# Kernel optimization log

Hardware: AMD Instinct MI355X
Metric: run time of the kernel (lower is better)

## Reference

```python
import jax, jax.numpy as jnp
import numpy as np

B, P, ENC = 128, 196, 2048
A, E, H = 512, 512, 512
V, TMAX = 20000, 20


def setup_inputs() -> dict:
    key = jax.random.key(0)
    ks = jax.random.split(key, 16)
    s = 0.02
    img = jax.random.normal(ks[0], (B, P, ENC), jnp.float32)
    cap = jax.random.randint(ks[1], (B, TMAX), 0, V)
    # ensure max(caplen) == TMAX so output shapes are deterministic
    caplen = jnp.concatenate([jnp.array([TMAX]),
                              jax.random.randint(ks[2], (B - 1,), 5, TMAX + 1)])
    emb = s * jax.random.normal(ks[3], (V, E), jnp.float32)
    We = s * jax.random.normal(ks[4], (ENC, A), jnp.float32)
    be = jnp.zeros((A,), jnp.float32)
    Wd = s * jax.random.normal(ks[5], (H, A), jnp.float32)
    bd = jnp.zeros((A,), jnp.float32)
    Wf = s * jax.random.normal(ks[6], (A, 1), jnp.float32)
    bf = jnp.zeros((1,), jnp.float32)
    W_ih = s * jax.random.normal(ks[7], (3 * H, E + ENC), jnp.float32)
    b_ih = jnp.zeros((3 * H,), jnp.float32)
    W_hh = s * jax.random.normal(ks[8], (3 * H, H), jnp.float32)
    b_hh = jnp.zeros((3 * H,), jnp.float32)
    Wo = s * jax.random.normal(ks[9], (V, H), jnp.float32)
    bo = jnp.zeros((V,), jnp.float32)
    return dict(img=img, cap=cap, caplen=caplen, emb=emb, We=We, be=be,
                Wd=Wd, bd=bd, Wf=Wf, bf=bf, W_ih=W_ih, b_ih=b_ih,
                W_hh=W_hh, b_hh=b_hh, Wo=Wo, bo=bo)


def reference(img, cap, caplen, emb, We, be, Wd, bd, Wf, bf,
              W_ih, b_ih, W_hh, b_hh, Wo, bo):
    T = int(np.asarray(jnp.max(caplen)))  # static loop length (caplen.tolist() in torch)
    word_emb = emb[cap]                       # [B, TMAX, E]
    att1 = jnp.einsum('bpe,ea->bpa', img, We) + be  # encoder attention, hoisted (img is constant over steps)

    def step(h, x_t):
        att2 = h @ Wd + bd                    # [B, A]
        fatt = jax.nn.relu(att1 + att2[:, None, :])   # [B, P, A]
        scores = fatt @ Wf + bf               # [B, P, 1]
        alpha = jax.nn.softmax(scores, axis=1)        # softmax over pixels
        ctx = jnp.sum(alpha * img, axis=1)    # [B, ENC]
        x = jnp.concatenate([x_t, ctx], axis=1)       # [B, E+ENC]
        gi = x @ W_ih.T + b_ih                # [B, 3H]
        gh = h @ W_hh.T + b_hh
        r = jax.nn.sigmoid(gi[:, :H] + gh[:, :H])
        z = jax.nn.sigmoid(gi[:, H:2 * H] + gh[:, H:2 * H])
        n = jnp.tanh(gi[:, 2 * H:] + r * gh[:, 2 * H:])
        h_new = (1.0 - z) * n + z * h
        preds = h_new @ Wo.T + bo             # [B, V]
        return h_new, (preds, alpha[..., 0])

    h0 = jnp.zeros((B, H), jnp.float32)
    xs = jnp.swapaxes(word_emb[:, :T - 1, :], 0, 1)   # [T-1, B, E]; step i uses word_emb[:, i-1]
    _, (preds_seq, alpha_seq) = jax.lax.scan(step, h0, xs)

    predictions = jnp.zeros((B, T, V), jnp.float32)
    predictions = predictions.at[:, 1:, :].set(jnp.swapaxes(preds_seq, 0, 1))
    predictions = predictions.at[:, 0, 1].set(1.0)
    alphas = jnp.zeros((B, T, P), jnp.float32)
    alphas = alphas.at[:, 1:, :].set(jnp.swapaxes(alpha_seq, 0, 1))
    return predictions, caplen, alphas
```

## Files before the change

### kernel.cpp

```cpp
#include <hip/hip_runtime.h>
#include <hip/hip_bf16.h>

#define B_    128
#define P_    196
#define ENC_  2048
#define A_    512
#define E_    512
#define H_    512
#define V_    20000
#define TMAX_ 20

#define CAPLEN_OFF 51200000L
#define ALPHA_OFF  51200128L

typedef __attribute__((ext_vector_type(4))) float f32x4;
typedef __attribute__((ext_vector_type(8))) short bf16x8;

#define GLL16(gsrc, ldst) \
  __builtin_amdgcn_global_load_lds((__attribute__((address_space(1))) const void*)(gsrc), \
                                   (__attribute__((address_space(3))) void*)(ldst), 16, 0, 0)

__device__ __forceinline__ unsigned short f2b(float x) {
  union { float f; unsigned u; } v; v.f = x;
  unsigned r = v.u + 0x7FFF + ((v.u >> 16) & 1);
  return (unsigned short)(r >> 16);
}
__device__ __forceinline__ float b2f(unsigned short u) {
  union { unsigned u; float f; } v; v.u = ((unsigned)u) << 16; return v.f;
}

__global__ __launch_bounds__(256) void k_setup(const int* __restrict__ caplen,
                                               float* __restrict__ out,
                                               float* __restrict__ h,
                                               unsigned short* __restrict__ h_bf) {
  long idx = (long)blockIdx.x * 256 + threadIdx.x;
  if (idx < (long)B_ * V_) {
    long b = idx / V_, v = idx % V_;
    out[b * (long)TMAX_ * V_ + v] = (v == 1) ? 1.0f : 0.0f;
  }
  if (idx < B_) out[CAPLEN_OFF + idx] = (float)caplen[idx];
  if (idx < (long)B_ * P_) {
    long b = idx / P_, p = idx % P_;
    out[ALPHA_OFF + b * (long)(TMAX_ * P_) + p] = 0.0f;
  }
  if (idx < B_ * H_) { h[idx] = 0.0f; h_bf[idx] = 0; }
}

__global__ __launch_bounds__(256) void k_cvt_t(const float* __restrict__ src,
                                               unsigned short* __restrict__ dst,
                                               int R, int C) {
  __shared__ float tile[32][33];
  int lx = threadIdx.x & 31, ly = threadIdx.x >> 5;
  int r0 = blockIdx.x * 32, c0 = blockIdx.y * 32;
#pragma unroll
  for (int j = 0; j < 32; j += 8)
    tile[ly + j][lx] = src[(long)(r0 + ly + j) * C + c0 + lx];
  __syncthreads();
#pragma unroll
  for (int j = 0; j < 32; j += 8)
    dst[(long)(c0 + ly + j) * R + r0 + lx] = f2b(tile[lx][ly + j]);
}

__global__ __launch_bounds__(256) void k_cvt_wo(const float* __restrict__ Wo,
                                                unsigned short* __restrict__ Wo_bf) {
  long gid = (long)blockIdx.x * 256 + threadIdx.x;
  long base = gid * 8;
  if (base >= (long)20096 * 512) return;
  long row = base >> 9;
  bf16x8 u;
  if (row < V_) {
    float4 f0 = *(const float4*)(Wo + base);
    float4 f1 = *(const float4*)(Wo + base + 4);
    u[0] = (short)f2b(f0.x); u[1] = (short)f2b(f0.y);
    u[2] = (short)f2b(f0.z); u[3] = (short)f2b(f0.w);
    u[4] = (short)f2b(f1.x); u[5] = (short)f2b(f1.y);
    u[6] = (short)f2b(f1.z); u[7] = (short)f2b(f1.w);
  } else {
    for (int j = 0; j < 8; ++j) u[j] = 0;
  }
  *(bf16x8*)(Wo_bf + base) = u;
}

__global__ __launch_bounds__(256) void k_cvt_img(const float* __restrict__ img,
                                                 unsigned short* __restrict__ img_bf) {
  long base = ((long)blockIdx.x * 256 + threadIdx.x) * 8;
  float4 f0 = *(const float4*)(img + base);
  float4 f1 = *(const float4*)(img + base + 4);
  bf16x8 u;
  u[0] = (short)f2b(f0.x); u[1] = (short)f2b(f0.y);
  u[2] = (short)f2b(f0.z); u[3] = (short)f2b(f0.w);
  u[4] = (short)f2b(f1.x); u[5] = (short)f2b(f1.y);
  u[6] = (short)f2b(f1.z); u[7] = (short)f2b(f1.w);
  *(bf16x8*)(img_bf + base) = u;
}

__global__ __launch_bounds__(256) void k_mfma_nt(const unsigned short* __restrict__ Abf,
                                                 const unsigned short* __restrict__ Bbf,
                                                 const float* __restrict__ bias,
                                                 float* __restrict__ C, long ldc,
                                                 int N, int K) {
  __shared__ unsigned short As[4096];
  __shared__ unsigned short Bs[4096];
  int tid = threadIdx.x, wave = tid >> 6, lane = tid & 63;
  int m0 = blockIdx.x * 128, n0 = blockIdx.y * 128;
  int wm = (wave & 1) * 64, wn = (wave >> 1) * 64;
  int rowL = tid >> 2, chkL = (tid & 3) * 8;
  const unsigned short* gA0 = Abf + (long)(m0 + rowL) * K + chkL;
  const unsigned short* gA1 = gA0 + (long)64 * K;
  const unsigned short* gB0 = Bbf + (long)(n0 + rowL) * K + chkL;
  const unsigned short* gB1 = gB0 + (long)64 * K;
  unsigned short* ldsA = As + wave * 512;
  unsigned short* ldsB = Bs + wave * 512;

  f32x4 acc[4][4];
#pragma unroll
  for (int i = 0; i < 4; ++i)
#pragma unroll
    for (int j = 0; j < 4; ++j) acc[i][j] = (f32x4){0.f, 0.f, 0.f, 0.f};

  int fm = lane & 15, q8 = (lane >> 4) * 8;
  for (int kc = 0; kc < K; kc += 32) {
    GLL16(gA0 + kc, ldsA);
    GLL16(gA1 + kc, ldsA + 2048);
    GLL16(gB0 + kc, ldsB);
    GLL16(gB1 + kc, ldsB + 2048);
    __syncthreads();
    bf16x8 af[4], bfr[4];
#pragma unroll
    for (int i = 0; i < 4; ++i)
      af[i] = *(const bf16x8*)&As[(wm + i * 16 + fm) * 32 + q8];
#pragma unroll
    for (int j = 0; j < 4; ++j)
      bfr[j] = *(const bf16x8*)&Bs[(wn + j * 16 + fm) * 32 + q8];
#pragma unroll
    for (int i = 0; i < 4; ++i)
#pragma unroll
      for (int j = 0; j < 4; ++j)
        acc[i][j] = __builtin_amdgcn_mfma_f32_16x16x32_bf16(af[i], bfr[j], acc[i][j], 0, 0, 0);
    __syncthreads();
  }
  int q4 = (lane >> 4) * 4;
#pragma unroll
  for (int i = 0; i < 4; ++i)
#pragma unroll
    for (int j = 0; j < 4; ++j) {
      int n = n0 + wn + j * 16 + fm;
      if (n < N) {
        float bv = bias[n];
#pragma unroll
        for (int r = 0; r < 4; ++r) {
          long m = m0 + wm + i * 16 + q4 + r;
          C[m * ldc + n] = acc[i][j][r] + bv;
        }
      }
    }
}

__global__ __launch_bounds__(256) void k_mfma_att1(const float* __restrict__ Aimg,
                                                   const unsigned short* __restrict__ Bbf,
                                                   const float* __restrict__ bias,
                                                   unsigned short* __restrict__ C) {
  __shared__ unsigned short As[4096];
  __shared__ unsigned short Bs[4096];
  int tid = threadIdx.x, wave = tid >> 6, lane = tid & 63;
  int m0 = blockIdx.x * 128, n0 = blockIdx.y * 128;
  int wm = (wave & 1) * 64, wn = (wave >> 1) * 64;
  int rowA = tid >> 1, segA = (tid & 1) * 16;
  const float* gA = Aimg + (long)(m0 + rowA) * ENC_ + segA;
  int rowL = tid >> 2, chkL = (tid & 3) * 8;
  const unsigned short* gB0 = Bbf + (long)(n0 + rowL) * ENC_ + chkL;
  const unsigned short* gB1 = gB0 + (long)64 * ENC_;
  unsigned short* ldsB = Bs + wave * 512;

  f32x4 acc[4][4];
#pragma unroll
  for (int i = 0; i < 4; ++i)
#pragma unroll
    for (int j = 0; j < 4; ++j) acc[i][j] = (f32x4){0.f, 0.f, 0.f, 0.f};

  int fm = lane & 15, q8 = (lane >> 4) * 8;
  for (int kc = 0; kc < ENC_; kc += 32) {
    GLL16(gB0 + kc, ldsB);
    GLL16(gB1 + kc, ldsB + 2048);
    float4 f0 = *(const float4*)(gA + kc);
    float4 f1 = *(const float4*)(gA + kc + 4);
    float4 f2 = *(const float4*)(gA + kc + 8);
    float4 f3 = *(const float4*)(gA + kc + 12);
    bf16x8 u0, u1;
    u0[0] = (short)f2b(f0.x); u0[1] = (short)f2b(f0.y);
    u0[2] = (short)f2b(f0.z); u0[3] = (short)f2b(f0.w);
    u0[4] = (short)f2b(f1.x); u0[5] = (short)f2b(f1.y);
    u0[6] = (short)f2b(f1.z); u0[7] = (short)f2b(f1.w);
    u1[0] = (short)f2b(f2.x); u1[1] = (short)f2b(f2.y);
    u1[2] = (short)f2b(f2.z); u1[3] = (short)f2b(f2.w);
    u1[4] = (short)f2b(f3.x); u1[5] = (short)f2b(f3.y);
    u1[6] = (short)f2b(f3.z); u1[7] = (short)f2b(f3.w);
    *(bf16x8*)&As[rowA * 32 + segA] = u0;
    *(bf16x8*)&As[rowA * 32 + segA + 8] = u1;
    __syncthreads();
    bf16x8 af[4], bfr[4];
#pragma unroll
    for (int i = 0; i < 4; ++i)
      af[i] = *(const bf16x8*)&As[(wm + i * 16 + fm) * 32 + q8];
#pragma unroll
    for (int j = 0; j < 4; ++j)
      bfr[j] = *(const bf16x8*)&Bs[(wn + j * 16 + fm) * 32 + q8];
#pragma unroll
    for (int i = 0; i < 4; ++i)
#pragma unroll
      for (int j = 0; j < 4; ++j)
        acc[i][j] = __builtin_amdgcn_mfma_f32_16x16x32_bf16(af[i], bfr[j], acc[i][j], 0, 0, 0);
    __syncthreads();
  }
  int q4 = (lane >> 4) * 4;
#pragma unroll
  for (int i = 0; i < 4; ++i)
#pragma unroll
    for (int j = 0; j < 4; ++j) {
      int n = n0 + wn + j * 16 + fm;
      float bv = bias[n];
#pragma unroll
      for (int r = 0; r < 4; ++r) {
        long m = m0 + wm + i * 16 + q4 + r;
        C[m * 512 + n] = f2b(acc[i][j][r] + bv);
      }
    }
}

__global__ __launch_bounds__(256) void k_attn_score(const unsigned short* __restrict__ att1_bf,
                                                    const float* __restrict__ att2,
                                                    const float* __restrict__ Wf,
                                                    const float* __restrict__ bfp,
                                                    float* __restrict__ alpha_ws,
                                                    float* __restrict__ out_alpha,
                                                    int t) {
  int b = blockIdx.x, tid = threadIdx.x;
  int wave = tid >> 6, lane = tid & 63;
  __shared__ float sc[P_ + 4];
  __shared__ float red[8];

  float a2[8], w8[8];
  {
    const float* ap = att2 + (long)b * 512 + lane * 8;
    float4 x0 = *(const float4*)ap, x1 = *(const float4*)(ap + 4);
    a2[0] = x0.x; a2[1] = x0.y; a2[2] = x0.z; a2[3] = x0.w;
    a2[4] = x1.x; a2[5] = x1.y; a2[6] = x1.z; a2[7] = x1.w;
    const float* wp = Wf + lane * 8;
    float4 y0 = *(const float4*)wp, y1 = *(const float4*)(wp + 4);
    w8[0] = y0.x; w8[1] = y0.y; w8[2] = y0.z; w8[3] = y0.w;
    w8[4] = y1.x; w8[5] = y1.y; w8[6] = y1.z; w8[7] = y1.w;
  }
  float bias0 = bfp[0];

  for (int p = wave; p < P_; p += 4) {
    bf16x8 v = *(const bf16x8*)(att1_bf + ((long)(b * P_ + p)) * 512 + lane * 8);
    float part = 0.f;
#pragma unroll
    for (int j = 0; j < 8; ++j) {
      float x = b2f((unsigned short)v[j]) + a2[j];
      part = fmaf(fmaxf(x, 0.f), w8[j], part);
    }
#pragma unroll
    for (int off = 32; off > 0; off >>= 1) part += __shfl_down(part, off);
    if (lane == 0) sc[p] = part + bias0;
  }
  __syncthreads();

  float mv = (tid < P_) ? sc[tid] : -1e30f;
#pragma unroll
  for (int off = 32; off > 0; off >>= 1) mv = fmaxf(mv, __shfl_down(mv, off));
  if (lane == 0) red[wave] = mv;
  __syncthreads();
  if (tid == 0) red[4] = fmaxf(fmaxf(red[0], red[1]), fmaxf(red[2], red[3]));
  __syncthreads();
  float mx = red[4];
  float e = (tid < P_) ? __expf(sc[tid] - mx) : 0.f;
  float sm = e;
#pragma unroll
  for (int off = 32; off > 0; off >>= 1) sm += __shfl_down(sm, off);
  if (lane == 0) red[wave] = sm;
  __syncthreads();
  if (tid == 0) red[5] = red[0] + red[1] + red[2] + red[3];
  __syncthreads();
  float inv = 1.f / red[5];
  if (tid < P_) {
    float al = e * inv;
    alpha_ws[b * P_ + tid] = al;
    out_alpha[((long)b * TMAX_ + t) * P_ + tid] = al;
  }
}

template <bool BFIMG>
__global__ __launch_bounds__(256) void k_attn_ctx(const void* __restrict__ img_v,
                                                  const float* __restrict__ alpha_ws,
                                                  float* __restrict__ ctx) {
  int b = blockIdx.x, ec = blockIdx.y;
  int tid = threadIdx.x, wave = tid >> 6, lane = tid & 63;
  __shared__ float als[P_];
  __shared__ float part[4][512];
  if (tid < P_) als[tid] = alpha_ws[b * P_ + tid];
  __syncthreads();
  float acc[8];
#pragma unroll
  for (int j = 0; j < 8; ++j) acc[j] = 0.f;
  long base = (long)b * P_ * ENC_ + ec * 512 + lane * 8;
  if (BFIMG) {
    const unsigned short* ib = (const unsigned short*)img_v;
    for (int p = wave; p < P_; p += 4) {
      float al = als[p];
      bf16x8 v = *(const bf16x8*)(ib + base + (long)p * ENC_);
#pragma unroll
      for (int j = 0; j < 8; ++j) acc[j] = fmaf(al, b2f((unsigned short)v[j]), acc[j]);
    }
  } else {
    const float* ip = (const float*)img_v;
    for (int p = wave; p < P_; p += 4) {
      float al = als[p];
      const float* r = ip + base + (long)p * ENC_;
      float4 v0 = *(const float4*)r, v1 = *(const float4*)(r + 4);
      acc[0] = fmaf(al, v0.x, acc[0]); acc[1] = fmaf(al, v0.y, acc[1]);
      acc[2] = fmaf(al, v0.z, acc[2]); acc[3] = fmaf(al, v0.w, acc[3]);
      acc[4] = fmaf(al, v1.x, acc[4]); acc[5] = fmaf(al, v1.y, acc[5]);
      acc[6] = fmaf(al, v1.z, acc[6]); acc[7] = fmaf(al, v1.w, acc[7]);
    }
  }
#pragma unroll
  for (int j = 0; j < 8; ++j) part[wave][lane * 8 + j] = acc[j];
  __syncthreads();
  for (int e = tid; e < 512; e += 256) {
    float s = part[0][e] + part[1][e] + part[2][e] + part[3][e];
    ctx[(long)b * ENC_ + ec * 512 + e] = s;
  }
}

__global__ __launch_bounds__(256) void k_gru_part(const float* __restrict__ emb,
                                                  const int* __restrict__ cap,
                                                  const float* __restrict__ ctx,
                                                  const float* __restrict__ h,
                                                  const float* __restrict__ W_ih,
                                                  const float* __restrict__ W_hh,
                                                  float* __restrict__ part,
                                                  int step) {
  __shared__ float As[128][68];
  __shared__ float Ws[32][68];
  int n0 = blockIdx.x * 32;
  int c  = blockIdx.y;
  int tid = threadIdx.x;
  int ng = tid & 7, mg = tid >> 3;

  float acc[4][4];
#pragma unroll
  for (int i = 0; i < 4; ++i)
#pragma unroll
    for (int j = 0; j < 4; ++j) acc[i][j] = 0.f;

  const float* Wbase;
  long wstride;
  if (c < 10) { Wbase = W_ih + (long)n0 * 2560 + c * 256;        wstride = 2560; }
  else        { Wbase = W_hh + (long)n0 * 512 + (c - 10) * 256;  wstride = 512;  }

  for (int s = 0; s < 4; ++s) {
    int ks = s * 64;
#pragma unroll
    for (int j = 0; j < 8; ++j) {
      int f = tid + j * 256;
      int r = f >> 4, kk = (f & 15) * 4;
      const float* src;
      if (c < 2)       src = emb + (long)cap[r * TMAX_ + step] * E_ + c * 256 + ks + kk;
      else if (c < 10) src = ctx + (long)r * ENC_ + (c - 2) * 256 + ks + kk;
      else             src = h   + (long)r * H_   + (c - 10) * 256 + ks + kk;
      *(float4*)&As[r][kk] = *(const float4*)src;
    }
#pragma unroll
    for (int j = 0; j < 2; ++j) {
      int f = tid + j * 256;
      int r = f >> 4, kk = (f & 15) * 4;
      *(float4*)&Ws[r][kk] = *(const float4*)(Wbase + (long)r * wstride + ks + kk);
    }
    __syncthreads();
#pragma unroll 4
    for (int k4 = 0; k4 < 16; ++k4) {
      float4 a[4], w[4];
#pragma unroll
      for (int i = 0; i < 4; ++i) a[i] = *(const float4*)&As[mg + 32 * i][k4 * 4];
#pragma unroll
      for (int j = 0; j < 4; ++j) w[j] = *(const float4*)&Ws[ng + 8 * j][k4 * 4];
#pragma unroll
      for (int i = 0; i < 4; ++i)
#pragma unroll
        for (int j = 0; j < 4; ++j)
          acc[i][j] = fmaf(a[i].x, w[j].x,
                      fmaf(a[i].y, w[j].y,
                      fmaf(a[i].z, w[j].z,
                      fmaf(a[i].w, w[j].w, acc[i][j]))));
    }
    __syncthreads();
  }

  float* dst = part + (long)c * (128 * 1536);
#pragma unroll
  for (int i = 0; i < 4; ++i) {
    int m = mg + 32 * i;
#pragma unroll
    for (int j = 0; j < 4; ++j)
      dst[(long)m * 1536 + n0 + ng + 8 * j] = acc[i][j];
  }
}

__global__ __launch_bounds__(256) void k_gate2(const float* __restrict__ part,
                                               const float* __restrict__ b_ih,
                                               const float* __restrict__ b_hh,
                                               float* __restrict__ h,
                                               unsigned short* __restrict__ h_bf) {
  int idx = blockIdx.x * 256 + threadIdx.x;
  int b = idx >> 9, j = idx & 511;
  long o = (long)b * 1536 + j;
  const long PS = 128L * 1536;
  float gir = 0.f, giz = 0.f, gin = 0.f;
  float ghr = 0.f, ghz = 0.f, ghn = 0.f;
#pragma unroll
  for (int c = 0; c < 10; ++c) {
    gir += part[c * PS + o];
    giz += part[c * PS + o + 512];
    gin += part[c * PS + o + 1024];
  }
#pragma unroll
  for (int c = 10; c < 12; ++c) {
    ghr += part[c * PS + o];
    ghz += part[c * PS + o + 512];
    ghn += part[c * PS + o + 1024];
  }
  gir += b_ih[j];        ghr += b_hh[j];
  giz += b_ih[j + 512];  ghz += b_hh[j + 512];
  gin += b_ih[j + 1024]; ghn += b_hh[j + 1024];
  float r = 1.f / (1.f + __expf(-(gir + ghr)));
  float z = 1.f / (1.f + __expf(-(giz + ghz)));
  float nn = tanhf(gin + r * ghn);
  float hv = h[idx];
  float v = (1.f - z) * nn + z * hv;
  h[idx] = v;
  h_bf[idx] = f2b(v);
}

__global__ __launch_bounds__(256) void k_gru_gemm(const float* __restrict__ emb,
                                                  const int* __restrict__ cap,
                                                  const float* __restrict__ ctx,
                                                  const float* __restrict__ h,
                                                  const float* __restrict__ W_ih,
                                                  const float* __restrict__ b_ih,
                                                  const float* __restrict__ W_hh,
                                                  const float* __restrict__ b_hh,
                                                  float* __restrict__ gi,
                                                  float* __restrict__ gh,
                                                  int step) {
  __shared__ float As[32][256];
  int m0 = blockIdx.x * 32;
  int n0 = blockIdx.y * 64;
  int tid = threadIdx.x;
  int np = tid & 31, slot = tid >> 5;
  int n = n0 + np * 2;
  float ai[4][2], ah[4][2];
#pragma unroll
  for (int i = 0; i < 4; ++i) { ai[i][0] = ai[i][1] = ah[i][0] = ah[i][1] = 0.f; }

  for (int c = 0; c < 10; ++c) {
#pragma unroll
    for (int j = 0; j < 8; ++j) {
      int f = tid + j * 256;
      int r = f >> 6, k = (f & 63) * 4;
      int bb = m0 + r;
      const float* src;
      if (c < 2) src = emb + (long)cap[bb * TMAX_ + step] * E_ + c * 256 + k;
      else       src = ctx + (long)bb * ENC_ + (c - 2) * 256 + k;
      *(float4*)&As[r][k] = *(const float4*)src;
    }
    __syncthreads();
    const float* W0 = W_ih + (long)n * 2560 + c * 256;
    const float* W1 = W0 + 2560;
#pragma unroll 4
    for (int k4 = 0; k4 < 64; ++k4) {
      float4 b0 = *(const float4*)&W0[k4 * 4];
      float4 b1 = *(const float4*)&W1[k4 * 4];
#pragma unroll
      for (int i = 0; i < 4; ++i) {
        float4 a = *(const float4*)&As[slot * 4 + i][k4 * 4];
        ai[i][0] = fmaf(a.x, b0.x, fmaf(a.y, b0.y, fmaf(a.z, b0.z, fmaf(a.w, b0.w, ai[i][0]))));
        ai[i][1] = fmaf(a.x, b1.x, fmaf(a.y, b1.y, fmaf(a.z, b1.z, fmaf(a.w, b1.w, ai[i][1]))));
      }
    }
    __syncthreads();
  }
  for (int c = 0; c < 2; ++c) {
#pragma unroll
    for (int j = 0; j < 8; ++j) {
      int f = tid + j * 256;
      int r = f >> 6, k = (f & 63) * 4;
      int bb = m0 + r;
      *(float4*)&As[r][k] = *(const float4*)&h[(long)bb * H_ + c * 256 + k];
    }
    __syncthreads();
    const float* W0 = W_hh + (long)n * 512 + c * 256;
    const float* W1 = W0 + 512;
#pragma unroll 4
    for (int k4 = 0; k4 < 64; ++k4) {
      float4 b0 = *(const float4*)&W0[k4 * 4];
      float4 b1 = *(const float4*)&W1[k4 * 4];
#pragma unroll
      for (int i = 0; i < 4; ++i) {
        float4 a = *(const float4*)&As[slot * 4 + i][k4 * 4];
        ah[i][0] = fmaf(a.x, b0.x, fmaf(a.y, b0.y, fmaf(a.z, b0.z, fmaf(a.w, b0.w, ah[i][0]))));
        ah[i][1] = fmaf(a.x, b1.x, fmaf(a.y, b1.y, fmaf(a.z, b1.z, fmaf(a.w, b1.w, ah[i][1]))));
      }
    }
    __syncthreads();
  }
#pragma unroll
  for (int i = 0; i < 4; ++i) {
    long m = m0 + slot * 4 + i;
    gi[m * 1536 + n]     = ai[i][0] + b_ih[n];
    gi[m * 1536 + n + 1] = ai[i][1] + b_ih[n + 1];
    gh[m * 1536 + n]     = ah[i][0] + b_hh[n];
    gh[m * 1536 + n + 1] = ah[i][1] + b_hh[n + 1];
  }
}

__global__ __launch_bounds__(256) void k_gate(const float* __restrict__ gi,
                                              const float* __restrict__ gh,
                                              float* __restrict__ h,
                                              unsigned short* __restrict__ h_bf) {
  int idx = blockIdx.x * 256 + threadIdx.x;
  int b = idx >> 9, j = idx & 511;
  long o = (long)b * 1536 + j;
  float r = 1.f / (1.f + __expf(-(gi[o] + gh[o])));
  float z = 1.f / (1.f + __expf(-(gi[o + 512] + gh[o + 512])));
  float nn = tanhf(gi[o + 1024] + r * gh[o + 1024]);
  float hv = h[idx];
  float v = (1.f - z) * nn + z * hv;
  h[idx] = v;
  h_bf[idx] = f2b(v);
}

extern "C" void kernel_launch(void* const* d_in, const int* in_sizes, int n_in,
                              void* d_out, int out_size, void* d_ws, size_t ws_size,
                              hipStream_t stream) {
  const float* img    = (const float*)d_in[0];
  const int*   cap    = (const int*)d_in[1];
  const int*   caplen = (const int*)d_in[2];
  const float* emb    = (const float*)d_in[3];
  const float* We     = (const float*)d_in[4];
  const float* be     = (const float*)d_in[5];
  const float* Wd     = (const float*)d_in[6];
  const float* bd     = (const float*)d_in[7];
  const float* Wf     = (const float*)d_in[8];
  const float* bfp    = (const float*)d_in[9];
  const float* W_ih   = (const float*)d_in[10];
  const float* b_ih   = (const float*)d_in[11];
  const float* W_hh   = (const float*)d_in[12];
  const float* b_hh   = (const float*)d_in[13];
  const float* Wo     = (const float*)d_in[14];
  const float* bo     = (const float*)d_in[15];
  float* out = (float*)d_out;
  char*  W   = (char*)d_ws;

  unsigned short* att1_bf = (unsigned short*)(W + 0);
  unsigned short* WeT_bf  = (unsigned short*)(W + 25690112);
  unsigned short* WdT_bf  = (unsigned short*)(W + 27787264);
  unsigned short* Wo_bf   = (unsigned short*)(W + 28311552);
  float*          h       = (float*)(W + 48889856);
  unsigned short* h_bf    = (unsigned short*)(W + 49152000);
  float*          ctx     = (float*)(W + 49283072);
  float*          gi      = (float*)(W + 50331648);
  float*          gh      = (float*)(W + 51118080);
  float*          att2    = (float*)(W + 51904512);
  float*          alpha_w = (float*)(W + 52166656);
  unsigned short* img_bf  = (unsigned short*)(W + 52267008);
  float*          part    = (float*)(W + 155027456);
  bool use_bfimg = ws_size >= 155027456ULL;
  bool use_part  = ws_size >= 164464640ULL;

  k_setup<<<10000, 256, 0, stream>>>(caplen, out, h, h_bf);
  k_cvt_t<<<dim3(64, 16), 256, 0, stream>>>(We, WeT_bf, ENC_, A_);
  k_cvt_t<<<dim3(16, 16), 256, 0, stream>>>(Wd, WdT_bf, H_, A_);
  k_cvt_wo<<<5024, 256, 0, stream>>>(Wo, Wo_bf);
  if (use_bfimg) k_cvt_img<<<25088, 256, 0, stream>>>(img, img_bf);
  k_mfma_att1<<<dim3(196, 4), 256, 0, stream>>>(img, WeT_bf, be, att1_bf);

  for (int i = 0; i < TMAX_ - 1; ++i) {
    int t = i + 1;
    k_mfma_nt<<<dim3(1, 4), 256, 0, stream>>>(h_bf, WdT_bf, bd, att2, 512, 512, 512);
    k_attn_score<<<128, 256, 0, stream>>>(att1_bf, att2, Wf, bfp, alpha_w,
                                          out + ALPHA_OFF, t);
    if (use_bfimg)
      k_attn_ctx<true><<<dim3(128, 4), 256, 0, stream>>>(img_bf, alpha_w, ctx);
    else
      k_attn_ctx<false><<<dim3(128, 4), 256, 0, stream>>>(img, alpha_w, ctx);
    if (use_part) {
      k_gru_part<<<dim3(48, 12), 256, 0, stream>>>(emb, cap, ctx, h, W_ih, W_hh,
                                                   part, i);
      k_gate2<<<256, 256, 0, stream>>>(part, b_ih, b_hh, h, h_bf);
    } else {
      k_gru_gemm<<<dim3(4, 24), 256, 0, stream>>>(emb, cap, ctx, h, W_ih, b_ih,
                                                  W_hh, b_hh, gi, gh, i);
      k_gate<<<256, 256, 0, stream>>>(gi, gh, h, h_bf);
    }
    k_mfma_nt<<<dim3(1, 157), 256, 0, stream>>>(h_bf, Wo_bf, bo,
                                                out + (long)t * V_,
                                                (long)TMAX_ * V_, V_, 512);
  }
}
```

Baseline: 2.871 ms.

## Split attention context over pixel chunks with atomics; reuse bf16 GEMM for att1

The attention-context kernel now splits the 196 pixels into 7 chunks of 28. Each block accumulates its partial context and adds it into ctx with atomics. ctx is zeroed inside the score kernel, so more blocks are in flight and no per-block shared-memory reduction is needed. When the bf16 image copy exists, the att1 projection now runs through the generic bf16 GEMM with a templated bf16 output instead of the kernel that converts fp32 on the fly. The fallback GRU gemm/gate path, which lacked the partial-sum workspace, is removed. The changes risk atomic contention, nondeterministic summation order, and breakage when the workspace is too small for the partial buffer.

```diff
diff --git a/kernel.cpp b/kernel.cpp
--- a/kernel.cpp
+++ b/kernel.cpp
@@ -94,10 +94,11 @@
   *(bf16x8*)(img_bf + base) = u;
 }
 
-__global__ __launch_bounds__(256) void k_mfma_nt(const unsigned short* __restrict__ Abf,
+template <int OBF>
+__global__ __launch_bounds__(256) void k_gemm_nt(const unsigned short* __restrict__ Abf,
                                                  const unsigned short* __restrict__ Bbf,
                                                  const float* __restrict__ bias,
-                                                 float* __restrict__ C, long ldc,
+                                                 void* __restrict__ Cv, long ldc,
                                                  int N, int K) {
   __shared__ unsigned short As[4096];
   __shared__ unsigned short Bs[4096];
@@ -146,11 +147,12 @@
     for (int j = 0; j < 4; ++j) {
       int n = n0 + wn + j * 16 + fm;
       if (n < N) {
-        float bv = bias[n];
+        float bv = bias ? bias[n] : 0.f;
 #pragma unroll
         for (int r = 0; r < 4; ++r) {
           long m = m0 + wm + i * 16 + q4 + r;
-          C[m * ldc + n] = acc[i][j][r] + bv;
+          if (OBF) ((unsigned short*)Cv)[m * ldc + n] = f2b(acc[i][j][r] + bv);
+          else     ((float*)Cv)[m * ldc + n] = acc[i][j][r] + bv;
         }
       }
     }
@@ -233,11 +235,19 @@
                                                     const float* __restrict__ bfp,
                                                     float* __restrict__ alpha_ws,
                                                     float* __restrict__ out_alpha,
+                                                    float* __restrict__ ctx,
                                                     int t) {
   int b = blockIdx.x, tid = threadIdx.x;
   int wave = tid >> 6, lane = tid & 63;
   __shared__ float sc[P_ + 4];
   __shared__ float red[8];
+
+  {
+    float4 z4 = {0.f, 0.f, 0.f, 0.f};
+    float* c = ctx + (long)b * ENC_ + tid * 8;
+    *(float4*)c = z4;
+    *(float4*)(c + 4) = z4;
+  }
 
   float a2[8], w8[8];
   {
@@ -290,8 +300,31 @@
   }
 }
 
-template <bool BFIMG>
-__global__ __launch_bounds__(256) void k_attn_ctx(const void* __restrict__ img_v,
+__global__ __launch_bounds__(256) void k_attn_ctx2(const unsigned short* __restrict__ img_bf,
+                                                   const float* __restrict__ alpha_ws,
+                                                   float* __restrict__ ctx) {
+  int b = blockIdx.x, pc = blockIdx.y;
+  int tid = threadIdx.x;
+  __shared__ float als[28];
+  if (tid < 28) als[tid] = alpha_ws[b * P_ + pc * 28 + tid];
+  __syncthreads();
+  float acc[8];
+#pragma unroll
+  for (int j = 0; j < 8; ++j) acc[j] = 0.f;
+  const unsigned short* base = img_bf + ((long)b * P_ + pc * 28) * ENC_ + tid * 8;
+#pragma unroll 4
+  for (int p = 0; p < 28; ++p) {
+    bf16x8 v = *(const bf16x8*)(base + (long)p * ENC_);
+    float al = als[p];
+#pragma unroll
+    for (int j = 0; j < 8; ++j) acc[j] = fmaf(al, b2f((unsigned short)v[j]), acc[j]);
+  }
+  float* c = ctx + (long)b * ENC_ + tid * 8;
+#pragma unroll
+  for (int j = 0; j < 8; ++j) atomicAdd(c + j, acc[j]);
+}
+
+__global__ __launch_bounds__(256) void k_attn_ctx(const float* __restrict__ img,
                                                   const float* __restrict__ alpha_ws,
                                                   float* __restrict__ ctx) {
   int b = blockIdx.x, ec = blockIdx.y;
@@ -304,25 +337,14 @@
 #pragma unroll
   for (int j = 0; j < 8; ++j) acc[j] = 0.f;
   long base = (long)b * P_ * ENC_ + ec * 512 + lane * 8;
-  if (BFIMG) {
-    const unsigned short* ib = (const unsigned short*)img_v;
-    for (int p = wave; p < P_; p += 4) {
-      float al = als[p];
-      bf16x8 v = *(const bf16x8*)(ib + base + (long)p * ENC_);
-#pragma unroll
-      for (int j = 0; j < 8; ++j) acc[j] = fmaf(al, b2f((unsigned short)v[j]), acc[j]);
-    }
-  } else {
-    const float* ip = (const float*)img_v;
-    for (int p = wave; p < P_; p += 4) {
-      float al = als[p];
-      const float* r = ip + base + (long)p * ENC_;
-      float4 v0 = *(const float4*)r, v1 = *(const float4*)(r + 4);
-      acc[0] = fmaf(al, v0.x, acc[0]); acc[1] = fmaf(al, v0.y, acc[1]);
-      acc[2] = fmaf(al, v0.z, acc[2]); acc[3] = fmaf(al, v0.w, acc[3]);
-      acc[4] = fmaf(al, v1.x, acc[4]); acc[5] = fmaf(al, v1.y, acc[5]);
-      acc[6] = fmaf(al, v1.z, acc[6]); acc[7] = fmaf(al, v1.w, acc[7]);
-    }
+  for (int p = wave; p < P_; p += 4) {
+    float al = als[p];
+    const float* r = img + base + (long)p * ENC_;
+    float4 v0 = *(const float4*)r, v1 = *(const float4*)(r + 4);
+    acc[0] = fmaf(al, v0.x, acc[0]); acc[1] = fmaf(al, v0.y, acc[1]);
+    acc[2] = fmaf(al, v0.z, acc[2]); acc[3] = fmaf(al, v0.w, acc[3]);
+    acc[4] = fmaf(al, v1.x, acc[4]); acc[5] = fmaf(al, v1.y, acc[5]);
+    acc[6] = fmaf(al, v1.z, acc[6]); acc[7] = fmaf(al, v1.w, acc[7]);
   }
 #pragma unroll
   for (int j = 0; j < 8; ++j) part[wave][lane * 8 + j] = acc[j];
@@ -436,104 +458,6 @@
   float r = 1.f / (1.f + __expf(-(gir + ghr)));
   float z = 1.f / (1.f + __expf(-(giz + ghz)));
   float nn = tanhf(gin + r * ghn);
-  float hv = h[idx];
-  float v = (1.f - z) * nn + z * hv;
-  h[idx] = v;
-  h_bf[idx] = f2b(v);
-}
-
-__global__ __launch_bounds__(256) void k_gru_gemm(const float* __restrict__ emb,
-                                                  const int* __restrict__ cap,
-                                                  const float* __restrict__ ctx,
-                                                  const float* __restrict__ h,
-                                                  const float* __restrict__ W_ih,
-                                                  const float* __restrict__ b_ih,
-                                                  const float* __restrict__ W_hh,
-                                                  const float* __restrict__ b_hh,
-                                                  float* __restrict__ gi,
-                                                  float* __restrict__ gh,
-                                                  int step) {
-  __shared__ float As[32][256];
-  int m0 = blockIdx.x * 32;
-  int n0 = blockIdx.y * 64;
-  int tid = threadIdx.x;
-  int np = tid & 31, slot = tid >> 5;
-  int n = n0 + np * 2;
-  float ai[4][2], ah[4][2];
-#pragma unroll
-  for (int i = 0; i < 4; ++i) { ai[i][0] = ai[i][1] = ah[i][0] = ah[i][1] = 0.f; }
-
-  for (int c = 0; c < 10; ++c) {
-#pragma unroll
-    for (int j = 0; j < 8; ++j) {
-      int f = tid + j * 256;
-      int r = f >> 6, k = (f & 63) * 4;
-      int bb = m0 + r;
-      const float* src;
-      if (c < 2) src = emb + (long)cap[bb * TMAX_ + step] * E_ + c * 256 + k;
-      else       src = ctx + (long)bb * ENC_ + (c - 2) * 256 + k;
-      *(float4*)&As[r][k] = *(const float4*)src;
-    }
-    __syncthreads();
-    const float* W0 = W_ih + (long)n * 2560 + c * 256;
-    const float* W1 = W0 + 2560;
-#pragma unroll 4
-    for (int k4 = 0; k4 < 64; ++k4) {
-      float4 b0 = *(const float4*)&W0[k4 * 4];
-      float4 b1 = *(const float4*)&W1[k4 * 4];
-#pragma unroll
-      for (int i = 0; i < 4; ++i) {
-        float4 a = *(const float4*)&As[slot * 4 + i][k4 * 4];
-        ai[i][0] = fmaf(a.x, b0.x, fmaf(a.y, b0.y, fmaf(a.z, b0.z, fmaf(a.w, b0.w, ai[i][0]))));
-        ai[i][1] = fmaf(a.x, b1.x, fmaf(a.y, b1.y, fmaf(a.z, b1.z, fmaf(a.w, b1.w, ai[i][1]))));
-      }
-    }
-    __syncthreads();
-  }
-  for (int c = 0; c < 2; ++c) {
-#pragma unroll
-    for (int j = 0; j < 8; ++j) {
-      int f = tid + j * 256;
-      int r = f >> 6, k = (f & 63) * 4;
-      int bb = m0 + r;
-      *(float4*)&As[r][k] = *(const float4*)&h[(long)bb * H_ + c * 256 + k];
-    }
-    __syncthreads();
-    const float* W0 = W_hh + (long)n * 512 + c * 256;
-    const float* W1 = W0 + 512;
-#pragma unroll 4
-    for (int k4 = 0; k4 < 64; ++k4) {
-      float4 b0 = *(const float4*)&W0[k4 * 4];
-      float4 b1 = *(const float4*)&W1[k4 * 4];
-#pragma unroll
-      for (int i = 0; i < 4; ++i) {
-        float4 a = *(const float4*)&As[slot * 4 + i][k4 * 4];
-        ah[i][0] = fmaf(a.x, b0.x, fmaf(a.y, b0.y, fmaf(a.z, b0.z, fmaf(a.w, b0.w, ah[i][0]))));
-        ah[i][1] = fmaf(a.x, b1.x, fmaf(a.y, b1.y, fmaf(a.z, b1.z, fmaf(a.w, b1.w, ah[i][1]))));
-      }
-    }
-    __syncthreads();
-  }
-#pragma unroll
-  for (int i = 0; i < 4; ++i) {
-    long m = m0 + slot * 4 + i;
-    gi[m * 1536 + n]     = ai[i][0] + b_ih[n];
-    gi[m * 1536 + n + 1] = ai[i][1] + b_ih[n + 1];
-    gh[m * 1536 + n]     = ah[i][0] + b_hh[n];
-    gh[m * 1536 + n + 1] = ah[i][1] + b_hh[n + 1];
-  }
-}
-
-__global__ __launch_bounds__(256) void k_gate(const float* __restrict__ gi,
-                                              const float* __restrict__ gh,
-                                              float* __restrict__ h,
-                                              unsigned short* __restrict__ h_bf) {
-  int idx = blockIdx.x * 256 + threadIdx.x;
-  int b = idx >> 9, j = idx & 511;
-  long o = (long)b * 1536 + j;
-  float r = 1.f / (1.f + __expf(-(gi[o] + gh[o])));
-  float z = 1.f / (1.f + __expf(-(gi[o + 512] + gh[o + 512])));
-  float nn = tanhf(gi[o + 1024] + r * gh[o + 1024]);
   float hv = h[idx];
   float v = (1.f - z) * nn + z * hv;
   h[idx] = v;
@@ -569,8 +493,6 @@
   float*          h       = (float*)(W + 48889856);
   unsigned short* h_bf    = (unsigned short*)(W + 49152000);
   float*          ctx     = (float*)(W + 49283072);
-  float*          gi      = (float*)(W + 50331648);
-  float*          gh      = (float*)(W + 51118080);
   float*          att2    = (float*)(W + 51904512);
   float*          alpha_w = (float*)(W + 52166656);
   unsigned short* img_bf  = (unsigned short*)(W + 52267008);
@@ -582,29 +504,31 @@
   k_cvt_t<<<dim3(64, 16), 256, 0, stream>>>(We, WeT_bf, ENC_, A_);
   k_cvt_t<<<dim3(16, 16), 256, 0, stream>>>(Wd, WdT_bf, H_, A_);
   k_cvt_wo<<<5024, 256, 0, stream>>>(Wo, Wo_bf);
-  if (use_bfimg) k_cvt_img<<<25088, 256, 0, stream>>>(img, img_bf);
-  k_mfma_att1<<<dim3(196, 4), 256, 0, stream>>>(img, WeT_bf, be, att1_bf);
+  if (use_bfimg) {
+    k_cvt_img<<<25088, 256, 0, stream>>>(img, img_bf);
+    k_gemm_nt<1><<<dim3(196, 4), 256, 0, stream>>>(img_bf, WeT_bf, be,
+                                                   att1_bf, 512, 512, ENC_);
+  } else {
+    k_mfma_att1<<<dim3(196, 4), 256, 0, stream>>>(img, WeT_bf, be, att1_bf);
+  }
 
   for (int i = 0; i < TMAX_ - 1; ++i) {
     int t = i + 1;
-    k_mfma_nt<<<dim3(1, 4), 256, 0, stream>>>(h_bf, WdT_bf, bd, att2, 512, 512, 512);
+    k_gemm_nt<0><<<dim3(1, 4), 256, 0, stream>>>(h_bf, WdT_bf, bd,
+                                                 att2, 512, 512, 512);
     k_attn_score<<<128, 256, 0, stream>>>(att1_bf, att2, Wf, bfp, alpha_w,
-                                          out + ALPHA_OFF, t);
+                                          out + ALPHA_OFF, ctx, t);
     if (use_bfimg)
-      k_attn_ctx<true><<<dim3(128, 4), 256, 0, stream>>>(img_bf, alpha_w, ctx);
+      k_attn_ctx2<<<dim3(128, 7), 256, 0, stream>>>(img_bf, alpha_w, ctx);
     else
-      k_attn_ctx<false><<<dim3(128, 4), 256, 0, stream>>>(img, alpha_w, ctx);
+      k_attn_ctx<<<dim3(128, 4), 256, 0, stream>>>(img, alpha_w, ctx);
     if (use_part) {
       k_gru_part<<<dim3(48, 12), 256, 0, stream>>>(emb, cap, ctx, h, W_ih, W_hh,
                                                    part, i);
       k_gate2<<<256, 256, 0, stream>>>(part, b_ih, b_hh, h, h_bf);
-    } else {
-      k_gru_gemm<<<dim3(4, 24), 256, 0, stream>>>(emb, cap, ctx, h, W_ih, b_ih,
-                                                  W_hh, b_hh, gi, gh, i);
-      k_gate<<<256, 256, 0, stream>>>(gi, gh, h, h_bf);
-    }
-    k_mfma_nt<<<dim3(1, 157), 256, 0, stream>>>(h_bf, Wo_bf, bo,
-                                                out + (long)t * V_,
-                                                (long)TMAX_ * V_, V_, 512);
-  }
-}
+    }
+    k_gemm_nt<0><<<dim3(1, 157), 256, 0, stream>>>(h_bf, Wo_bf, bo,
+                                                   out + (long)t * V_,
+                                                   (long)TMAX_ * V_, V_, 512);
+  }
+}
```

Result: slower. 3.606 ms, median of 2 (+25.6%).
